# Kernel tuning notes

Hardware: AMD Instinct MI355X
Metric: run time of the kernel (lower is better)

Reference implementation:

```python
import jax, jax.numpy as jnp
import numpy as np

HO, WO = 64, 64
SHARPNESS = 150.0


def _stereographic_grid(ho, wo):
    # Matches create_normal_grid(..., 'stereographic'); torch.meshgrid 'ij':
    # v varies over rows (ho), u over cols (wo).
    v, u = np.meshgrid(np.arange(ho), np.arange(wo), indexing='ij')
    p = 4.0 * ((u + 0.5) / wo - 0.5)
    q = -4.0 * ((v + 0.5) / ho - 0.5)
    d = 1.0 + p ** 2 + q ** 2
    z = -(-1.0 + p ** 2 + q ** 2) / d
    m = (z > 0.0).astype(np.float32)
    x = 2.0 * p / d * m
    y = 2.0 * q / d * m
    z = z * m
    return np.stack([x, y, z], axis=-1).reshape(-1, 3).astype(np.float32)  # [ho*wo,3]


_GRID = _stereographic_grid(HO, WO)
_IDX = np.nonzero(np.any(_GRID != 0, axis=-1))[0]  # static valid-query indices [N]
_QN = _GRID[_IDX]  # [N,3]


def setup_inputs() -> dict:
    key = jax.random.key(0)
    k1, k2, k3 = jax.random.split(key, 3)
    bs, c, h, w = 2, 64, 192, 192
    in_fea_map = jax.random.normal(k1, (bs, c, h, w), dtype=jnp.float32)
    nrm = jax.random.normal(k2, (bs, 3, h, w), dtype=jnp.float32)
    in_normal_map = nrm / (jnp.linalg.norm(nrm, axis=1, keepdims=True) + 1e-8)
    in_mask_map = (jax.random.uniform(k3, (bs, 1, h, w)) > 0.2).astype(jnp.float32)
    log_query_norm = jnp.full((1,), np.log(SHARPNESS), dtype=jnp.float32)
    return {"in_fea_map": in_fea_map, "in_normal_map": in_normal_map,
            "in_mask_map": in_mask_map, "log_query_norm": log_query_norm}


def reference(in_fea_map, in_normal_map, in_mask_map, log_query_norm):
    bs, c, h, w = in_fea_map.shape
    hw = h * w
    qn = jnp.asarray(_QN, dtype=in_fea_map.dtype)  # [N,3] static valid queries
    vals = in_fea_map.reshape(bs, c, hw).transpose(0, 2, 1)       # [bs,HW,c]
    key_n = in_normal_map.reshape(bs, 3, hw)                       # [bs,3,HW]
    cos = jnp.einsum('nd,bdm->bnm', qn, key_n)                     # [bs,N,HW]
    dps = cos / np.float32(np.sqrt(3.0))
    dps = dps - jnp.max(dps, axis=-1, keepdims=True)
    w_ = jnp.exp(jnp.exp(log_query_norm) * dps)                    # dropout in eval = identity
    w_ = w_ * in_mask_map.reshape(bs, 1, hw)
    weights = w_ / (jnp.sum(w_, axis=-1, keepdims=True) + 1e-9)    # [bs,N,HW]
    mapped = weights @ vals                                        # [bs,N,c]
    mapped = jnp.concatenate([jnp.broadcast_to(qn, (bs,) + qn.shape), mapped], axis=-1)
    # variance map over last 3 feature channels
    mean = mapped[..., -3:]
    sq_mean = weights @ (vals[..., -3:] ** 2)
    var = jnp.sum(sq_mean - mean ** 2, axis=-1, keepdims=True)
    mapped = jnp.concatenate([var, mapped], axis=-1)
    # cosine map
    rm_cos = jnp.sum(weights * cos, axis=-1, keepdims=True)
    mapped = jnp.concatenate([rm_cos, mapped], axis=-1)            # [bs,N,c+5]
    C = mapped.shape[-1]
    out = jnp.zeros((bs, HO * WO, C), mapped.dtype).at[:, _IDX, :].set(mapped)
    return out.transpose(0, 2, 1).reshape(bs, C, HO, WO)
```

## Files before the change

kernel.cpp:

```cpp
#include <hip/hip_runtime.h>
#include <hip/hip_bf16.h>
#include <cstdint>
#include <cstddef>

#define HW 36864
#define QT 64
#define NCHA 69

constexpr bool is_valid_px(int v, int u) {
  int a = 2 * u - 63, b = 2 * v - 63;
  return a * a + b * b < 1024;
}
constexpr int count_valid() {
  int n = 0;
  for (int v = 0; v < 64; ++v)
    for (int u = 0; u < 64; ++u)
      if (is_valid_px(v, u)) ++n;
  return n;
}
constexpr int NV  = count_valid();
constexpr int NQT = (NV + QT - 1) / QT;
constexpr int NQP = NQT * QT;
constexpr int PLANE = 2 * NQP * NCHA;

struct QTab {
  short idx[NQP];
  short rank[4096];
};
constexpr QTab make_qtab() {
  QTab t{};
  int n = 0;
  for (int p = 0; p < 4096; ++p) {
    int v = p >> 6, u = p & 63;
    if (is_valid_px(v, u)) { t.idx[n] = (short)p; t.rank[p] = (short)n; ++n; }
    else t.rank[p] = -1;
  }
  for (int i = n; i < NQP; ++i) t.idx[i] = -1;
  return t;
}
__constant__ QTab g_qtab = make_qtab();

typedef short short8 __attribute__((ext_vector_type(8)));
typedef float f32x4  __attribute__((ext_vector_type(4)));

__device__ __forceinline__ unsigned short f2b(float f) {
  unsigned int u = __float_as_uint(f);
  u += 0x7FFFu + ((u >> 16) & 1u);
  return (unsigned short)(u >> 16);
}
__device__ __forceinline__ ushort2 f2b2(float a, float b) {
  __hip_bfloat162 h = __float22bfloat162_rn(make_float2(a, b));
  return *(ushort2*)&h;
}
__device__ __forceinline__ ushort4 f2b4(float4 v) {
  ushort4 r;
  *(ushort2*)&r.x = f2b2(v.x, v.y);
  *(ushort2*)&r.z = f2b2(v.z, v.w);
  return r;
}
__device__ __forceinline__ void pix2qn(int pix, float& x, float& y, float& z) {
  x = 0.f; y = 0.f; z = 0.f;
  if (pix >= 0) {
    int v = pix >> 6, u = pix & 63;
    float p = (float)(2 * u - 63) * (1.0f / 32.0f);
    float q = -(float)(2 * v - 63) * (1.0f / 32.0f);
    float d = 1.0f + p * p + q * q;
    x = 2.0f * p / d; y = 2.0f * q / d; z = (1.0f - p * p - q * q) / d;
  }
}


template<int KSC>
__global__ __launch_bounds__(128, 2) void partial_kernel(
    const float* __restrict__ fea,
    const float* __restrict__ nrm,
    const float* __restrict__ msk,
    const float* __restrict__ lqn,
    float* __restrict__ part)
{
  constexpr int SLICE  = HW / KSC;
  constexpr int NCHUNK = SLICE / 64;

  __shared__ __align__(16) unsigned short v_s[2][80][72];
  __shared__ __align__(16) float nrm4_s[2][64][4];
  __shared__ float ex_s[64][9];

  const int bx  = blockIdx.x;
  const int cls = bx & 7;
  const int r0  = bx >> 3;
  const int qt  = r0 % NQT;
  const int sh  = r0 / NQT;
  const int s   = sh * 8 + cls;
  const int b   = s / KSC;
  const int ks  = s % KSC;

  const int t    = threadIdx.x;
  const int wv   = t >> 6;
  const int l    = t & 63;
  const int lq   = l >> 4;
  const int mrow = l & 15;

  const float Cc = __expf(lqn[0]) * 0.57735026919f;

  float qx[2], qy[2], qz[2];
  pix2qn(g_qtab.idx[qt * QT + 32 * wv + mrow],      qx[0], qy[0], qz[0]);
  pix2qn(g_qtab.idx[qt * QT + 32 * wv + 16 + mrow], qx[1], qy[1], qz[1]);

  for (int s0 = t; s0 < 160; s0 += 128) {
    int row = 70 + (s0 >> 4);
    int p4  = (s0 & 15) * 4;
    unsigned short c = (row == 70) ? (unsigned short)0x3F80 : (unsigned short)0;
    ushort4 cv; cv.x = c; cv.y = c; cv.z = c; cv.w = c;
    *(ushort4*)&v_s[0][row][p4] = cv;
    *(ushort4*)&v_s[1][row][p4] = cv;
  }

  const size_t base_f = (size_t)b * 64 * HW;
  const size_t base_n = (size_t)b * 3 * HW;
  const size_t base_m = (size_t)b * HW;

  const int chb = t >> 4;
  const int px4 = (t & 15) * 4;
  const int pxp = 32 * (l >> 5) + 4 * (l & 7) + ((l >> 3) & 3);

  f32x4 acc[2][5];
  #pragma unroll
  for (int h = 0; h < 2; ++h)
    #pragma unroll
    for (int nt = 0; nt < 5; ++nt) acc[h][nt] = (f32x4)(0.0f);

  float4 pf[8];
  float pnA = 0.f, pnB = 0.f;

  auto load_chunk = [&](int ck) {
    int m0 = ks * SLICE + ck * 64;
    #pragma unroll
    for (int i = 0; i < 8; ++i)
      pf[i] = *(const float4*)(fea + base_f + (size_t)(chb + 8 * i) * HW + (size_t)(m0 + px4));
    pnA = nrm[base_n + (size_t)wv * HW + (size_t)(m0 + l)];
    pnB = (wv == 0) ? nrm[base_n + (size_t)2 * HW + (size_t)(m0 + l)]
                    : msk[base_m + (size_t)(m0 + l)];
  };
  auto store_chunk = [&](int buf) {
    #pragma unroll
    for (int i = 0; i < 8; ++i) {
      int ch = chb + 8 * i;
      float4 fv = pf[i];
      *(ushort4*)&v_s[buf][ch][px4] = f2b4(fv);
      if (ch >= 61) {
        float4 sq = make_float4(fv.x * fv.x, fv.y * fv.y, fv.z * fv.z, fv.w * fv.w);
        *(ushort4*)&v_s[buf][ch + 3][px4] = f2b4(sq);
      }
    }
    v_s[buf][67 + wv][l] = f2b(pnA);
    nrm4_s[buf][pxp][wv] = Cc * pnA;
    if (wv == 0) {
      v_s[buf][69][l] = f2b(pnB);
      nrm4_s[buf][pxp][2] = Cc * pnB;
    } else {
      nrm4_s[buf][pxp][3] = -Cc + (pnB > 0.5f ? 0.f : -2000.f);
    }
  };

  load_chunk(0);
  store_chunk(0);
  __syncthreads();

  for (int ck = 0; ck < NCHUNK; ++ck) {
    const int buf = ck & 1;
    if (ck + 1 < NCHUNK) load_chunk(ck + 1);

    #pragma unroll
    for (int kk = 0; kk < 64; kk += 32) {
      float e0[8], e1[8];
      #pragma unroll
      for (int j = 0; j < 8; ++j) {
        const float4 nv = *(const float4*)&nrm4_s[buf][kk + 4 * j + lq][0];
        float t0 = fmaf(qx[0], nv.x, fmaf(qy[0], nv.y, fmaf(qz[0], nv.z, nv.w)));
        float t1 = fmaf(qx[1], nv.x, fmaf(qy[1], nv.y, fmaf(qz[1], nv.z, nv.w)));
        e0[j] = __expf(t0);
        e1[j] = __expf(t1);
      }
      short8 a0, a1;
      #pragma unroll
      for (int p = 0; p < 4; ++p) {
        ushort2 p0 = f2b2(e0[2 * p], e0[2 * p + 1]);
        ushort2 p1 = f2b2(e1[2 * p], e1[2 * p + 1]);
        a0[2 * p] = (short)p0.x; a0[2 * p + 1] = (short)p0.y;
        a1[2 * p] = (short)p1.x; a1[2 * p + 1] = (short)p1.y;
      }
      #pragma unroll
      for (int nt = 0; nt < 5; ++nt) {
        short8 bb = *(const short8*)&v_s[buf][16 * nt + mrow][kk + 8 * lq];
        acc[0][nt] = __builtin_amdgcn_mfma_f32_16x16x32_bf16(a0, bb, acc[0][nt], 0, 0, 0);
        acc[1][nt] = __builtin_amdgcn_mfma_f32_16x16x32_bf16(a1, bb, acc[1][nt], 0, 0, 0);
      }
    }

    if (ck + 1 < NCHUNK) {
      store_chunk(buf ^ 1);
      __syncthreads();
    }
  }

  const size_t pbase = (size_t)ks * PLANE + ((size_t)b * NQP + (size_t)(qt * QT)) * NCHA;
  #pragma unroll
  for (int h = 0; h < 2; ++h) {
    #pragma unroll
    for (int nt = 0; nt < 4; ++nt) {
      #pragma unroll
      for (int rr = 0; rr < 4; ++rr) {
        int qloc = 32 * wv + 16 * h + 4 * lq + rr;
        part[pbase + (size_t)qloc * NCHA + (size_t)(16 * nt + mrow)] = acc[h][nt][rr];
      }
    }
    if (mrow < 7) {
      #pragma unroll
      for (int rr = 0; rr < 4; ++rr)
        ex_s[32 * wv + 16 * h + 4 * lq + rr][mrow] = acc[h][4][rr];
    }
  }
  __syncthreads();
  if (t < 64) {
    float gx, gy, gz;
    pix2qn(g_qtab.idx[qt * QT + t], gx, gy, gz);
    float swc = gx * ex_s[t][3] + gy * ex_s[t][4] + gz * ex_s[t][5];
    size_t o = pbase + (size_t)t * NCHA;
    part[o + 64] = ex_s[t][0];
    part[o + 65] = ex_s[t][1];
    part[o + 66] = ex_s[t][2];
    part[o + 67] = swc;
    part[o + 68] = ex_s[t][6];
  }
}

#define NFIN (2 * NQT * 8)
#define NTAIL (2 * NFIN)

__global__ __launch_bounds__(256) void finalize_kernel(
    const float* __restrict__ part,
    float* __restrict__ out,
    int ksc)
{
  const int blk = blockIdx.x;
  const int t   = threadIdx.x;

  if (blk < NFIN) {
    __shared__ float sm[8][NCHA];
    const int b   = blk / (NQT * 8);
    const int rem = blk % (NQT * 8);
    const int qt  = rem >> 3;
    const int qr  = rem & 7;
    const int q0  = qt * QT + qr * 8;

    const size_t colbase = ((size_t)b * NQP + (size_t)q0) * NCHA;
    for (int i = t; i < 8 * NCHA; i += 256) {
      float sv = 0.f;
      const size_t off = colbase + (size_t)i;
      #pragma unroll 8
      for (int k = 0; k < ksc; ++k) sv += part[(size_t)k * PLANE + off];
      sm[0][i] = sv;
    }
    __syncthreads();

    for (int i = t; i < 8 * NCHA; i += 256) {
      const int ql = i / NCHA;
      const int oc = i % NCHA;
      const int pix = g_qtab.idx[q0 + ql];
      if (pix < 0) continue;
      const float* A = sm[ql];
      const float inv = 1.0f / (A[68] + 1e-9f);
      float gx, gy, gz;
      pix2qn(pix, gx, gy, gz);
      float val;
      if (oc == 0)      val = A[67] * inv;
      else if (oc == 1) {
        val = 0.f;
        #pragma unroll
        for (int j = 0; j < 3; ++j) {
          float m  = A[61 + j] * inv;
          float sq = A[64 + j] * inv;
          val += sq - m * m;
        }
      }
      else if (oc == 2) val = gx;
      else if (oc == 3) val = gy;
      else if (oc == 4) val = gz;
      else              val = A[oc - 5] * inv;
      out[((size_t)b * NCHA + (size_t)oc) * 4096 + pix] = val;
    }
  } else {
    const int start = (blk - NFIN) * 256 + t;
    const int strd  = (NTAIL - NFIN) * 256;
    const int TOT   = 2 * NCHA * 4096;
    for (int i = start; i < TOT; i += strd) {
      if (g_qtab.rank[i & 4095] < 0) out[i] = 0.0f;
    }
  }
}

extern "C" void kernel_launch(void* const* d_in, const int* in_sizes, int n_in,
                              void* d_out, int out_size, void* d_ws, size_t ws_size,
                              hipStream_t stream) {
  const float* fea = (const float*)d_in[0];
  const float* nrm = (const float*)d_in[1];
  const float* msk = (const float*)d_in[2];
  const float* lqn = (const float*)d_in[3];
  float* part = (float*)d_ws;
  float* out  = (float*)d_out;

  const size_t need32 = (size_t)PLANE * 32 * sizeof(float);
  if (ws_size >= need32) {
    partial_kernel<32><<<dim3(2 * 32 * NQT), 128, 0, stream>>>(fea, nrm, msk, lqn, part);
    finalize_kernel<<<dim3(NTAIL), 256, 0, stream>>>(part, out, 32);
  } else {
    partial_kernel<16><<<dim3(2 * 16 * NQT), 128, 0, stream>>>(fea, nrm, msk, lqn, part);
    finalize_kernel<<<dim3(NTAIL), 256, 0, stream>>>(part, out, 16);
  }
}
```

Before: 121.2 us.

## Split K across four waves per block and raise split-K count to 64

The partial kernel now runs 256 threads per block. Each pair of waves takes one half of each 64-pixel chunk in K, and the two halves are reduced through shared memory at the end. Loads per thread drop from eight float4 to four. When the workspace is large enough, the split-K factor rises to 64, so more blocks run. The cost is an extra LDS reduction, more partial-sum traffic for the finalize kernel to read, and higher register pressure under the tighter launch bounds.

```diff
diff --git a/kernel.cpp b/kernel.cpp
--- a/kernel.cpp
+++ b/kernel.cpp
@@ -71,7 +71,7 @@
 
 
 template<int KSC>
-__global__ __launch_bounds__(128, 2) void partial_kernel(
+__global__ __launch_bounds__(256, 4) void partial_kernel(
     const float* __restrict__ fea,
     const float* __restrict__ nrm,
     const float* __restrict__ msk,
@@ -83,7 +83,6 @@
 
   __shared__ __align__(16) unsigned short v_s[2][80][72];
   __shared__ __align__(16) float nrm4_s[2][64][4];
-  __shared__ float ex_s[64][9];
 
   const int bx  = blockIdx.x;
   const int cls = bx & 7;
@@ -96,6 +95,8 @@
 
   const int t    = threadIdx.x;
   const int wv   = t >> 6;
+  const int Mh   = wv & 1;
+  const int kko  = (wv >> 1) * 32;
   const int l    = t & 63;
   const int lq   = l >> 4;
   const int mrow = l & 15;
@@ -103,12 +104,12 @@
   const float Cc = __expf(lqn[0]) * 0.57735026919f;
 
   float qx[2], qy[2], qz[2];
-  pix2qn(g_qtab.idx[qt * QT + 32 * wv + mrow],      qx[0], qy[0], qz[0]);
-  pix2qn(g_qtab.idx[qt * QT + 32 * wv + 16 + mrow], qx[1], qy[1], qz[1]);
-
-  for (int s0 = t; s0 < 160; s0 += 128) {
-    int row = 70 + (s0 >> 4);
-    int p4  = (s0 & 15) * 4;
+  pix2qn(g_qtab.idx[qt * QT + 32 * Mh + mrow],      qx[0], qy[0], qz[0]);
+  pix2qn(g_qtab.idx[qt * QT + 32 * Mh + 16 + mrow], qx[1], qy[1], qz[1]);
+
+  if (t < 160) {
+    int row = 70 + (t >> 4);
+    int p4  = (t & 15) * 4;
     unsigned short c = (row == 70) ? (unsigned short)0x3F80 : (unsigned short)0;
     ushort4 cv; cv.x = c; cv.y = c; cv.z = c; cv.w = c;
     *(ushort4*)&v_s[0][row][p4] = cv;
@@ -121,6 +122,7 @@
 
   const int chb = t >> 4;
   const int px4 = (t & 15) * 4;
+  const int arr = t >> 6;
   const int pxp = 32 * (l >> 5) + 4 * (l & 7) + ((l >> 3) & 3);
 
   f32x4 acc[2][5];
@@ -129,22 +131,21 @@
     #pragma unroll
     for (int nt = 0; nt < 5; ++nt) acc[h][nt] = (f32x4)(0.0f);
 
-  float4 pf[8];
-  float pnA = 0.f, pnB = 0.f;
+  float4 pf[4];
+  float pn = 0.f, pm = 0.f;
 
   auto load_chunk = [&](int ck) {
     int m0 = ks * SLICE + ck * 64;
     #pragma unroll
-    for (int i = 0; i < 8; ++i)
-      pf[i] = *(const float4*)(fea + base_f + (size_t)(chb + 8 * i) * HW + (size_t)(m0 + px4));
-    pnA = nrm[base_n + (size_t)wv * HW + (size_t)(m0 + l)];
-    pnB = (wv == 0) ? nrm[base_n + (size_t)2 * HW + (size_t)(m0 + l)]
-                    : msk[base_m + (size_t)(m0 + l)];
+    for (int i = 0; i < 4; ++i)
+      pf[i] = *(const float4*)(fea + base_f + (size_t)(chb + 16 * i) * HW + (size_t)(m0 + px4));
+    if (arr < 3) pn = nrm[base_n + (size_t)arr * HW + (size_t)(m0 + l)];
+    else         pm = msk[base_m + (size_t)(m0 + l)];
   };
   auto store_chunk = [&](int buf) {
     #pragma unroll
-    for (int i = 0; i < 8; ++i) {
-      int ch = chb + 8 * i;
+    for (int i = 0; i < 4; ++i) {
+      int ch = chb + 16 * i;
       float4 fv = pf[i];
       *(ushort4*)&v_s[buf][ch][px4] = f2b4(fv);
       if (ch >= 61) {
@@ -152,13 +153,11 @@
         *(ushort4*)&v_s[buf][ch + 3][px4] = f2b4(sq);
       }
     }
-    v_s[buf][67 + wv][l] = f2b(pnA);
-    nrm4_s[buf][pxp][wv] = Cc * pnA;
-    if (wv == 0) {
-      v_s[buf][69][l] = f2b(pnB);
-      nrm4_s[buf][pxp][2] = Cc * pnB;
+    if (arr < 3) {
+      v_s[buf][67 + arr][l] = f2b(pn);
+      nrm4_s[buf][pxp][arr] = Cc * pn;
     } else {
-      nrm4_s[buf][pxp][3] = -Cc + (pnB > 0.5f ? 0.f : -2000.f);
+      nrm4_s[buf][pxp][3] = -Cc + (pm > 0.5f ? 0.f : -2000.f);
     }
   };
 
@@ -170,31 +169,28 @@
     const int buf = ck & 1;
     if (ck + 1 < NCHUNK) load_chunk(ck + 1);
 
-    #pragma unroll
-    for (int kk = 0; kk < 64; kk += 32) {
-      float e0[8], e1[8];
-      #pragma unroll
-      for (int j = 0; j < 8; ++j) {
-        const float4 nv = *(const float4*)&nrm4_s[buf][kk + 4 * j + lq][0];
-        float t0 = fmaf(qx[0], nv.x, fmaf(qy[0], nv.y, fmaf(qz[0], nv.z, nv.w)));
-        float t1 = fmaf(qx[1], nv.x, fmaf(qy[1], nv.y, fmaf(qz[1], nv.z, nv.w)));
-        e0[j] = __expf(t0);
-        e1[j] = __expf(t1);
-      }
-      short8 a0, a1;
-      #pragma unroll
-      for (int p = 0; p < 4; ++p) {
-        ushort2 p0 = f2b2(e0[2 * p], e0[2 * p + 1]);
-        ushort2 p1 = f2b2(e1[2 * p], e1[2 * p + 1]);
-        a0[2 * p] = (short)p0.x; a0[2 * p + 1] = (short)p0.y;
-        a1[2 * p] = (short)p1.x; a1[2 * p + 1] = (short)p1.y;
-      }
-      #pragma unroll
-      for (int nt = 0; nt < 5; ++nt) {
-        short8 bb = *(const short8*)&v_s[buf][16 * nt + mrow][kk + 8 * lq];
-        acc[0][nt] = __builtin_amdgcn_mfma_f32_16x16x32_bf16(a0, bb, acc[0][nt], 0, 0, 0);
-        acc[1][nt] = __builtin_amdgcn_mfma_f32_16x16x32_bf16(a1, bb, acc[1][nt], 0, 0, 0);
-      }
+    float e0[8], e1[8];
+    #pragma unroll
+    for (int j = 0; j < 8; ++j) {
+      const float4 nv = *(const float4*)&nrm4_s[buf][kko + 4 * j + lq][0];
+      float t0 = fmaf(qx[0], nv.x, fmaf(qy[0], nv.y, fmaf(qz[0], nv.z, nv.w)));
+      float t1 = fmaf(qx[1], nv.x, fmaf(qy[1], nv.y, fmaf(qz[1], nv.z, nv.w)));
+      e0[j] = __expf(t0);
+      e1[j] = __expf(t1);
+    }
+    short8 a0, a1;
+    #pragma unroll
+    for (int p = 0; p < 4; ++p) {
+      ushort2 p0 = f2b2(e0[2 * p], e0[2 * p + 1]);
+      ushort2 p1 = f2b2(e1[2 * p], e1[2 * p + 1]);
+      a0[2 * p] = (short)p0.x; a0[2 * p + 1] = (short)p0.y;
+      a1[2 * p] = (short)p1.x; a1[2 * p + 1] = (short)p1.y;
+    }
+    #pragma unroll
+    for (int nt = 0; nt < 5; ++nt) {
+      short8 bb = *(const short8*)&v_s[buf][16 * nt + mrow][kko + 8 * lq];
+      acc[0][nt] = __builtin_amdgcn_mfma_f32_16x16x32_bf16(a0, bb, acc[0][nt], 0, 0, 0);
+      acc[1][nt] = __builtin_amdgcn_mfma_f32_16x16x32_bf16(a1, bb, acc[1][nt], 0, 0, 0);
     }
 
     if (ck + 1 < NCHUNK) {
@@ -203,34 +199,59 @@
     }
   }
 
+  __syncthreads();
+  float* scr = (float*)&v_s[0][0][0];
+  float* exs = scr + 64 * 80;
+
+  if (kko) {
+    #pragma unroll
+    for (int h = 0; h < 2; ++h)
+      #pragma unroll
+      for (int nt = 0; nt < 5; ++nt)
+        #pragma unroll
+        for (int rr = 0; rr < 4; ++rr) {
+          int qloc = 32 * Mh + 16 * h + 4 * lq + rr;
+          scr[qloc * 80 + 16 * nt + mrow] = acc[h][nt][rr];
+        }
+  }
+  __syncthreads();
   const size_t pbase = (size_t)ks * PLANE + ((size_t)b * NQP + (size_t)(qt * QT)) * NCHA;
-  #pragma unroll
-  for (int h = 0; h < 2; ++h) {
-    #pragma unroll
-    for (int nt = 0; nt < 4; ++nt) {
+  if (!kko) {
+    #pragma unroll
+    for (int h = 0; h < 2; ++h) {
       #pragma unroll
-      for (int rr = 0; rr < 4; ++rr) {
-        int qloc = 32 * wv + 16 * h + 4 * lq + rr;
-        part[pbase + (size_t)qloc * NCHA + (size_t)(16 * nt + mrow)] = acc[h][nt][rr];
+      for (int nt = 0; nt < 5; ++nt)
+        #pragma unroll
+        for (int rr = 0; rr < 4; ++rr) {
+          int qloc = 32 * Mh + 16 * h + 4 * lq + rr;
+          acc[h][nt][rr] += scr[qloc * 80 + 16 * nt + mrow];
+        }
+      #pragma unroll
+      for (int nt = 0; nt < 4; ++nt)
+        #pragma unroll
+        for (int rr = 0; rr < 4; ++rr) {
+          int qloc = 32 * Mh + 16 * h + 4 * lq + rr;
+          part[pbase + (size_t)qloc * NCHA + (size_t)(16 * nt + mrow)] = acc[h][nt][rr];
+        }
+      if (mrow < 7) {
+        #pragma unroll
+        for (int rr = 0; rr < 4; ++rr)
+          exs[(32 * Mh + 16 * h + 4 * lq + rr) * 9 + mrow] = acc[h][4][rr];
       }
-    }
-    if (mrow < 7) {
-      #pragma unroll
-      for (int rr = 0; rr < 4; ++rr)
-        ex_s[32 * wv + 16 * h + 4 * lq + rr][mrow] = acc[h][4][rr];
     }
   }
   __syncthreads();
   if (t < 64) {
     float gx, gy, gz;
     pix2qn(g_qtab.idx[qt * QT + t], gx, gy, gz);
-    float swc = gx * ex_s[t][3] + gy * ex_s[t][4] + gz * ex_s[t][5];
+    const float* E = exs + t * 9;
+    float swc = gx * E[3] + gy * E[4] + gz * E[5];
     size_t o = pbase + (size_t)t * NCHA;
-    part[o + 64] = ex_s[t][0];
-    part[o + 65] = ex_s[t][1];
-    part[o + 66] = ex_s[t][2];
+    part[o + 64] = E[0];
+    part[o + 65] = E[1];
+    part[o + 66] = E[2];
     part[o + 67] = swc;
-    part[o + 68] = ex_s[t][6];
+    part[o + 68] = E[6];
   }
 }
 
@@ -309,12 +330,16 @@
   float* part = (float*)d_ws;
   float* out  = (float*)d_out;
 
+  const size_t need64 = (size_t)PLANE * 64 * sizeof(float);
   const size_t need32 = (size_t)PLANE * 32 * sizeof(float);
-  if (ws_size >= need32) {
-    partial_kernel<32><<<dim3(2 * 32 * NQT), 128, 0, stream>>>(fea, nrm, msk, lqn, part);
+  if (ws_size >= need64) {
+    partial_kernel<64><<<dim3(2 * 64 * NQT), 256, 0, stream>>>(fea, nrm, msk, lqn, part);
+    finalize_kernel<<<dim3(NTAIL), 256, 0, stream>>>(part, out, 64);
+  } else if (ws_size >= need32) {
+    partial_kernel<32><<<dim3(2 * 32 * NQT), 256, 0, stream>>>(fea, nrm, msk, lqn, part);
     finalize_kernel<<<dim3(NTAIL), 256, 0, stream>>>(part, out, 32);
   } else {
-    partial_kernel<16><<<dim3(2 * 16 * NQT), 128, 0, stream>>>(fea, nrm, msk, lqn, part);
+    partial_kernel<16><<<dim3(2 * 16 * NQT), 256, 0, stream>>>(fea, nrm, msk, lqn, part);
     finalize_kernel<<<dim3(NTAIL), 256, 0, stream>>>(part, out, 16);
   }
 }
```

After: 118.9 us. About the same (-1.9%).
